# Optimization experiments

Measured on AMD Instinct MI355X. Metric: run time of the kernel, lower is better.

Reference implementation:

```python
import jax, jax.numpy as jnp
import numpy as np

B, L, H, N, NLAYERS = 16, 2048, 256, 64, 4
PRENORM = True


def layer_norm(z, scale, bias, eps=1e-5):
    # z: (B, L, H); normalize over last (feature) axis
    mu = jnp.mean(z, axis=-1, keepdims=True)
    var = jnp.var(z, axis=-1, keepdims=True)
    return (z - mu) * jax.lax.rsqrt(var + eps) * scale + bias


def s4_block(u, log_dt, Alog, Aim, Cre, Cim, D, Wout, bout):
    # u: (B, H, L) -- canonical S4D block: FFT conv + D skip + GELU + GLU linear
    Lq = u.shape[-1]
    dt = jnp.exp(log_dt)[:, None]                      # (H, 1)
    A = -jnp.exp(Alog) + 1j * Aim                      # (H, N)
    C = Cre + 1j * Cim                                 # (H, N)
    dtA = A * dt                                       # (H, N)
    Cd = C * (jnp.exp(dtA) - 1.0) / A                  # ZOH discretization
    vand = jnp.exp(dtA[:, :, None] * jnp.arange(Lq))   # (H, N, L) Vandermonde
    K = 2.0 * jnp.real(jnp.einsum('hn,hnl->hl', Cd, vand))  # (H, L) conv kernel
    n = 2 * Lq
    y = jnp.fft.irfft(jnp.fft.rfft(u, n=n) * jnp.fft.rfft(K, n=n), n=n)[..., :Lq]
    y = y + D[:, None] * u
    y = jax.nn.gelu(y)
    z = jnp.einsum('oh,bhl->bol', Wout, y) + bout[None, :, None]  # (B, 2H, L)
    z1, z2 = jnp.split(z, 2, axis=1)
    return z1 * jax.nn.sigmoid(z2)                     # GLU -> (B, H, L)


def setup_inputs() -> dict:
    key = jax.random.key(0)
    ks = jax.random.split(key, 8)
    x = jax.random.normal(ks[0], (B, L, H), jnp.float32)
    # dt log-uniform in [1e-3, 1e-1]
    log_dt = jnp.log(10.0 ** jax.random.uniform(ks[1], (NLAYERS, H), minval=-3.0, maxval=-1.0)).astype(jnp.float32)
    Alog = jnp.log(0.5 * jnp.ones((NLAYERS, H, N), jnp.float32))
    Aim = jnp.broadcast_to(np.pi * jnp.arange(N, dtype=jnp.float32), (NLAYERS, H, N)).copy()
    Cre = jax.random.normal(ks[2], (NLAYERS, H, N), jnp.float32) * (0.5 ** 0.5)
    Cim = jax.random.normal(ks[3], (NLAYERS, H, N), jnp.float32) * (0.5 ** 0.5)
    D = jax.random.normal(ks[4], (NLAYERS, H), jnp.float32)
    Wout = jax.random.normal(ks[5], (NLAYERS, 2 * H, H), jnp.float32) / jnp.sqrt(jnp.float32(H))
    bout = jnp.zeros((NLAYERS, 2 * H), jnp.float32)
    ln_scale = jnp.ones((NLAYERS, H), jnp.float32)
    ln_bias = jnp.zeros((NLAYERS, H), jnp.float32)
    return dict(x=x, log_dt=log_dt, Alog=Alog, Aim=Aim, Cre=Cre, Cim=Cim, D=D,
                Wout=Wout, bout=bout, ln_scale=ln_scale, ln_bias=ln_bias)


def reference(x, log_dt, Alog, Aim, Cre, Cim, D, Wout, bout, ln_scale, ln_bias):
    # x: (B, L, H); module transposes to (B, H, L) internally
    h = jnp.swapaxes(x, -1, -2)
    for i in range(NLAYERS):
        z = h
        if PRENORM:
            z = jnp.swapaxes(layer_norm(jnp.swapaxes(z, -1, -2), ln_scale[i], ln_bias[i]), -1, -2)
        z = s4_block(z, log_dt[i], Alog[i], Aim[i], Cre[i], Cim[i], D[i], Wout[i], bout[i])
        h = z + h  # dropout is identity in eval mode
        if not PRENORM:
            h = jnp.swapaxes(layer_norm(jnp.swapaxes(h, -1, -2), ln_scale[i], ln_bias[i]), -1, -2)
    return jnp.swapaxes(h, -1, -2)
```

## Files before the change

### kernel.cpp

```cpp
#include <hip/hip_runtime.h>
#include <hip/hip_bf16.h>
#include <math.h>

#define Bq 16
#define Lq 2048
#define Hq 256
#define Nst 64
#define LC 128
#define NC 16
#define NL 4
#define BC 256
#define GK 256
#define PWS 133
#define SZ ((size_t)Bq * Lq * Hq)

typedef __attribute__((ext_vector_type(8))) short short8;
typedef __attribute__((ext_vector_type(4))) float f32x4;
typedef unsigned short u16;
typedef unsigned int u32;

__device__ __forceinline__ u16 f2b(float x) {
  __hip_bfloat16 b = __float2bfloat16(x);
  u16 u; __builtin_memcpy(&u, &b, 2); return u;
}
__device__ __forceinline__ float b2f(u16 u) {
  u32 t = ((u32)u) << 16; float f; __builtin_memcpy(&f, &t, 4); return f;
}
__device__ __forceinline__ void gload16(const void* g, void* l) {
  __builtin_amdgcn_global_load_lds(
      (const __attribute__((address_space(1))) void*)g,
      (__attribute__((address_space(3))) void*)l, 16, 0, 0);
}

__global__ __launch_bounds__(256) void param_k(
    const float* __restrict__ log_dt, const float* __restrict__ Alog,
    const float* __restrict__ Aim, const float* __restrict__ Cre,
    const float* __restrict__ Cim, const float* __restrict__ Dv,
    u16* __restrict__ Vb, u16* __restrict__ TRb, float* __restrict__ wLc) {
  int lh = blockIdx.x;
  int tid = threadIdx.x;
  __shared__ float pwre[32][PWS], pwim[32][PWS];
  __shared__ float cdre[32], cdim[32];
  __shared__ float kacc[LC];
  __shared__ float kts[LC];
  int ln2 = tid & 31, pg = tid >> 5;
  float dlt = expf(log_dt[lh]);

  for (int pass = 0; pass < 2; ++pass) {
    int n = pass * 32 + ln2;
    int gi = lh * Nst + n;
    float ar = -expf(Alog[gi]);
    float ai = Aim[gi];
    float dr = ar * dlt, di = ai * dlt;
    float er = expf(dr); float sn, cs; sincosf(di, &sn, &cs);
    float wr = er * cs, wi = er * sn;
    float p0 = (float)(16 * pg);
    float eb = expf(dr * p0); float sb, cb; sincosf(di * p0, &sb, &cb);
    float pr = eb * cb, pi = eb * sb;
    #pragma unroll
    for (int s = 0; s < 16; ++s) {
      pwre[ln2][16*pg + s] = pr; pwim[ln2][16*pg + s] = pi;
      float t = pr*wr - pi*wi; pi = fmaf(pr, wi, pi*wr); pr = t;
    }
    if (pg == 7) {
      pwre[ln2][128] = pr; pwim[ln2][128] = pi;
      wLc[2*gi] = pr; wLc[2*gi+1] = pi;
    }
    if (pg == 0) {
      float nr = wr - 1.f, ni = wi;
      float d2 = ar*ar + ai*ai;
      float qr = (nr*ar + ni*ai) / d2;
      float qi = (ni*ar - nr*ai) / d2;
      float cr = Cre[gi], ci = Cim[gi];
      cdre[ln2] = cr*qr - ci*qi;
      cdim[ln2] = cr*qi + ci*qr;
    }
    __syncthreads();
    if (tid < LC) {
      float s = 0.f;
      #pragma unroll
      for (int k = 0; k < 32; ++k)
        s = fmaf(cdre[k], pwre[k][tid], fmaf(-cdim[k], pwim[k][tid], s));
      if (pass == 0) kacc[tid] = s;
      else kts[tid] = 2.f * (kacc[tid] + s) + ((tid == 0) ? Dv[lh] : 0.f);
    }
    #pragma unroll
    for (int it = 0; it < 32; ++it) {
      int idx = it * 256 + tid;
      int rl = idx >> 7, j = idx & 127;
      int nl = rl >> 1, im = rl & 1;
      int p = 127 - j;
      float v = im ? pwim[nl][p] : pwre[nl][p];
      Vb[((size_t)lh * 128 + 64*pass + rl) * 128 + j] = f2b(v);
    }
    #pragma unroll
    for (int it = 0; it < 32; ++it) {
      int idx = it * 256 + tid;
      int t = idx >> 6, rl = idx & 63;
      int nl = rl >> 1, im = rl & 1;
      float wpr = pwre[nl][t+1], wpi = pwim[nl][t+1];
      float qr = cdre[nl]*wpr - cdim[nl]*wpi;
      float qi = cdre[nl]*wpi + cdim[nl]*wpr;
      TRb[((size_t)lh * 128 + t) * 256 + 128 + 64*pass + rl] =
          f2b(im ? -2.f*qi : 2.f*qr);
    }
    __syncthreads();
  }
  #pragma unroll
  for (int it = 0; it < 64; ++it) {
    int idx = it * 256 + tid;
    int t = idx >> 7, j = idx & 127;
    TRb[((size_t)lh * 128 + t) * 256 + j] = f2b(j <= t ? kts[t - j] : 0.f);
  }
}

__global__ __launch_bounds__(256) void cvtw_k(
    const float* __restrict__ w, __hip_bfloat16* __restrict__ wb, int n) {
  int i = blockIdx.x * 256 + threadIdx.x;
  if (i < n) wb[i] = __float2bfloat16(w[i]);
}

__global__ __launch_bounds__(512) void lntr_k(
    const float* __restrict__ src, const float* __restrict__ sc,
    const float* __restrict__ bi, u16* __restrict__ zt) {
  int bc = blockIdx.x, jh = blockIdx.y;
  __shared__ u16 Lt[64][Hq + 6];
  int wave = threadIdx.x >> 6, lane = threadIdx.x & 63;
  float4 scv = ((const float4*)sc)[lane];
  float4 biv = ((const float4*)bi)[lane];
  #pragma unroll
  for (int rr = 0; rr < 8; ++rr) {
    int j = wave * 8 + rr;
    size_t row = (size_t)bc * LC + jh * 64 + j;
    const float4 v = ((const float4*)(src + row * Hq))[lane];
    float s  = v.x + v.y + v.z + v.w;
    float s2 = v.x*v.x + v.y*v.y + v.z*v.z + v.w*v.w;
    for (int off = 32; off; off >>= 1) { s += __shfl_down(s, off); s2 += __shfl_down(s2, off); }
    s = __shfl(s, 0); s2 = __shfl(s2, 0);
    float mu = s * (1.f / Hq);
    float var = s2 * (1.f / Hq) - mu * mu;
    float r = rsqrtf(var + 1e-5f);
    u32 w0 = (u32)f2b((v.x - mu) * r * scv.x + biv.x)
           | ((u32)f2b((v.y - mu) * r * scv.y + biv.y) << 16);
    u32 w1 = (u32)f2b((v.z - mu) * r * scv.z + biv.z)
           | ((u32)f2b((v.w - mu) * r * scv.w + biv.w) << 16);
    *(u32*)&Lt[j][4 * lane]     = w0;
    *(u32*)&Lt[j][4 * lane + 2] = w1;
  }
  __syncthreads();
  #pragma unroll
  for (int it = 0; it < 16; ++it) {
    int idx = it * 512 + threadIdx.x;
    int h = idx >> 5, jl = idx & 31;
    u32 lo = Lt[2*jl][h], hi = Lt[2*jl+1][h];
    ((u32*)zt)[((size_t)h * BC + bc) * 64 + jh * 32 + jl] = lo | (hi << 16);
  }
}

__global__ __launch_bounds__(512) void s4core_k(
    const u16* __restrict__ zt, const u16* __restrict__ Vb,
    const u16* __restrict__ TRb, const float* __restrict__ wLc,
    u16* __restrict__ ytb) {
  int h = blockIdx.y;
  int m0 = blockIdx.x * 128;
  __shared__ u16 As[2][128 * 64];
  __shared__ u16 Bs[128 * 64];
  int tid = threadIdx.x;
  int wid = tid >> 6, lane = tid & 63;
  int cl = lane & 15, kq = lane >> 4;
  int wm = wid & 1, wn = wid >> 1;

  const u16* Ab  = zt  + ((size_t)h * BC + m0) * 128;
  const u16* Vbb = Vb  + (size_t)h * 128 * 128;
  const u16* Tbb = TRb + (size_t)h * 128 * 256;

  #pragma unroll
  for (int half = 0; half < 2; ++half)
    #pragma unroll
    for (int q = 0; q < 2; ++q) {
      int idx = q * 512 + tid;
      int r = idx >> 3, ch = idx & 7;
      gload16(Ab + (size_t)r * 128 + half * 64 + ((ch ^ (r & 7)) << 3),
              (char*)As[half] + (size_t)(q * 512 + (tid & ~63)) * 16);
    }

  auto stageB = [&](const u16* base, int stride, int col0) {
    #pragma unroll
    for (int q = 0; q < 2; ++q) {
      int idx = q * 512 + tid;
      int r = idx >> 3, ch = idx & 7;
      gload16(base + (size_t)r * stride + col0 + ((ch ^ (r & 7)) << 3),
              (char*)Bs + (size_t)(q * 512 + (tid & ~63)) * 16);
    }
  };

  f32x4 accS[4][2] = {};
  f32x4 accY[4][2] = {};

  auto mfstep = [&](const u16* Asrc, f32x4 (*acc)[2]) {
    #pragma unroll
    for (int kk = 0; kk < 2; ++kk) {
      short8 a[4], bf[2];
      #pragma unroll
      for (int mi = 0; mi < 4; ++mi) {
        int m = wm * 64 + mi * 16 + cl;
        int ch = (kk * 4 + kq) ^ (m & 7);
        a[mi] = *(const short8*)(Asrc + m * 64 + ch * 8);
      }
      #pragma unroll
      for (int ni = 0; ni < 2; ++ni) {
        int n = wn * 32 + ni * 16 + cl;
        int ch = (kk * 4 + kq) ^ (n & 7);
        bf[ni] = *(const short8*)(Bs + n * 64 + ch * 8);
      }
      #pragma unroll
      for (int mi = 0; mi < 4; ++mi)
        #pragma unroll
        for (int ni = 0; ni < 2; ++ni)
          acc[mi][ni] = __builtin_amdgcn_mfma_f32_16x16x32_bf16(
              a[mi], bf[ni], acc[mi][ni], 0, 0, 0);
    }
  };

  stageB(Vbb, 128, 0);   __syncthreads();
  mfstep(As[0], accS);   __syncthreads();
  stageB(Vbb, 128, 64);  __syncthreads();
  mfstep(As[1], accS);   __syncthreads();
  stageB(Tbb, 256, 0);   __syncthreads();
  mfstep(As[0], accY);   __syncthreads();
  stageB(Tbb, 256, 64);  __syncthreads();
  mfstep(As[1], accY);

  float sgn = (cl & 1) ? 1.f : -1.f;
  #pragma unroll
  for (int ni = 0; ni < 2; ++ni) {
    int n = (wn * 32 + ni * 16 + cl) >> 1;
    float wr = wLc[2 * (h * Nst + n)];
    float wi = wLc[2 * (h * Nst + n) + 1];
    float swi = sgn * wi;
    #pragma unroll
    for (int mi = 0; mi < 4; ++mi) {
      float carry = 0.f;
      #pragma unroll
      for (int c = 0; c < NC; ++c) {
        float part = __shfl_xor(carry, 1);
        float a_used = accS[mi][ni][c & 3];
        float Sc = fmaf(wr, carry, fmaf(swi, part, a_used));
        if (kq == (c >> 2)) accS[mi][ni][c & 3] = carry;
        carry = __shfl(Sc, ((c >> 2) << 4) + cl);
      }
    }
  }

  __syncthreads();
  #pragma unroll
  for (int mi = 0; mi < 4; ++mi)
    #pragma unroll
    for (int ni = 0; ni < 2; ++ni) {
      int colv = wn * 32 + ni * 16 + cl;
      int half = colv >> 6, cv = colv & 63;
      #pragma unroll
      for (int r = 0; r < 4; ++r) {
        int m = wm * 64 + mi * 16 + kq * 4 + r;
        As[half][m * 64 + (((cv >> 3) ^ (m & 7)) << 3) + (cv & 7)] =
            f2b(accS[mi][ni][r]);
      }
    }
  stageB(Tbb, 256, 128);  __syncthreads();
  mfstep(As[0], accY);    __syncthreads();
  stageB(Tbb, 256, 192);  __syncthreads();
  mfstep(As[1], accY);

  #pragma unroll
  for (int mi = 0; mi < 4; ++mi)
    #pragma unroll
    for (int ni = 0; ni < 2; ++ni) {
      int t = wn * 32 + ni * 16 + cl;
      #pragma unroll
      for (int r = 0; r < 4; ++r) {
        int row = m0 + wm * 64 + mi * 16 + kq * 4 + r;
        float x = accY[mi][ni][r];
        float inner = 0.7978845608028654f * fmaf(0.044715f, x*x*x, x);
        float g = 0.5f * x * (1.f + tanhf(inner));
        ytb[((size_t)h * BC + row) * LC + t] = f2b(g);
      }
    }
}

__global__ __launch_bounds__(256) void trB_k(
    const u16* __restrict__ ytb, u16* __restrict__ ybb) {
  int bc = blockIdx.x;
  int h0 = blockIdx.y * 64;
  __shared__ float Lt[128][65];
  const u16* src = ytb + ((size_t)h0 * BC + bc) * LC;
  for (int it = 0; it < 16; ++it) {
    int idx = it * 256 + threadIdx.x;
    int hh = idx >> 6, tl = idx & 63;
    u32 v = *(const u32*)(src + (size_t)hh * BC * LC + 2 * tl);
    Lt[2*tl][hh]   = b2f((u16)(v & 0xffff));
    Lt[2*tl+1][hh] = b2f((u16)(v >> 16));
  }
  __syncthreads();
  for (int it = 0; it < 16; ++it) {
    int idx = it * 256 + threadIdx.x;
    int t = idx >> 5, hl = idx & 31;
    u32 lo = f2b(Lt[t][2*hl]);
    u32 hi = f2b(Lt[t][2*hl+1]);
    ((u32*)ybb)[((size_t)bc * LC + t) * (Hq / 2) + h0 / 2 + hl] = lo | (hi << 16);
  }
}

__global__ __launch_bounds__(256) void gemm_k(
    const __hip_bfloat16* __restrict__ ybb, const __hip_bfloat16* __restrict__ Wb,
    const float* __restrict__ bout, const float* __restrict__ rsrc,
    float* __restrict__ hb) {
  __shared__ __hip_bfloat16 As[128 * 64];
  __shared__ __hip_bfloat16 Bs[128 * 64];
  int tid = threadIdx.x;
  int m0 = blockIdx.x * 128;
  int ot = blockIdx.y;
  int wid = tid >> 6, lane = tid & 63;
  int cl = lane & 15, kq = lane >> 4;
  f32x4 acc[2][8] = {};
  for (int kt = 0; kt < GK / 64; ++kt) {
    int k0 = kt * 64;
    #pragma unroll
    for (int q = 0; q < 4; ++q) {
      int idx = q * 256 + tid;
      int r = idx >> 3, ch = idx & 7;
      const __hip_bfloat16* sA =
          ybb + (size_t)(m0 + r) * GK + k0 + ((ch ^ (r & 7)) << 3);
      gload16(sA, (char*)As + (size_t)(q * 256 + (tid & ~63)) * 16);
      int wrow = ot * 64 + r + ((r >= 64) ? 192 : 0);
      const __hip_bfloat16* sB =
          Wb + (size_t)wrow * GK + k0 + ((ch ^ (r & 7)) << 3);
      gload16(sB, (char*)Bs + (size_t)(q * 256 + (tid & ~63)) * 16);
    }
    __syncthreads();
    #pragma unroll
    for (int kk = 0; kk < 2; ++kk) {
      short8 a[2], bfr[8];
      #pragma unroll
      for (int mi = 0; mi < 2; ++mi) {
        int m = wid * 32 + mi * 16 + cl;
        int ch = (kk * 4 + kq) ^ (m & 7);
        a[mi] = *(const short8*)(As + m * 64 + ch * 8);
      }
      #pragma unroll
      for (int ni = 0; ni < 8; ++ni) {
        int n = ni * 16 + cl;
        int ch = (kk * 4 + kq) ^ (n & 7);
        bfr[ni] = *(const short8*)(Bs + n * 64 + ch * 8);
      }
      #pragma unroll
      for (int mi = 0; mi < 2; ++mi)
        #pragma unroll
        for (int ni = 0; ni < 8; ++ni)
          acc[mi][ni] = __builtin_amdgcn_mfma_f32_16x16x32_bf16(
              a[mi], bfr[ni], acc[mi][ni], 0, 0, 0);
    }
    __syncthreads();
  }
  #pragma unroll
  for (int mi = 0; mi < 2; ++mi) {
    #pragma unroll
    for (int ni = 0; ni < 4; ++ni) {
      int o1 = ot * 64 + ni * 16 + cl;
      float b1 = bout[o1], b2 = bout[o1 + 256];
      #pragma unroll
      for (int r = 0; r < 4; ++r) {
        int row = m0 + wid * 32 + mi * 16 + kq * 4 + r;
        float z1 = acc[mi][ni][r] + b1;
        float z2 = acc[mi][ni + 4][r] + b2;
        float g = z1 / (1.f + expf(-z2));
        size_t idx = (size_t)row * Hq + o1;
        hb[idx] = rsrc[idx] + g;
      }
    }
  }
}

extern "C" void kernel_launch(void* const* d_in, const int* in_sizes, int n_in,
                              void* d_out, int out_size, void* d_ws, size_t ws_size,
                              hipStream_t stream) {
  (void)in_sizes; (void)n_in; (void)out_size; (void)ws_size;
  const float* x      = (const float*)d_in[0];
  const float* log_dt = (const float*)d_in[1];
  const float* Alog   = (const float*)d_in[2];
  const float* Aim    = (const float*)d_in[3];
  const float* Cre    = (const float*)d_in[4];
  const float* Cim    = (const float*)d_in[5];
  const float* Dv     = (const float*)d_in[6];
  const float* Wout   = (const float*)d_in[7];
  const float* bout   = (const float*)d_in[8];
  const float* lns    = (const float*)d_in[9];
  const float* lnb    = (const float*)d_in[10];

  float* hb = (float*)d_out;
  float* p  = (float*)d_ws;
  u16* zt  = (u16*)p; p += SZ/2;
  u16* ytb = (u16*)p; p += SZ/2;
  u16* ybb = (u16*)p; p += SZ/2;
  u16* Vb  = (u16*)p; p += SZ;
  u16* TRb = (u16*)p; p += 2*SZ;
  u16* Wb  = (u16*)p; p += (NL*2*Hq*Hq)/2;
  float* wLc = p;  p += NL*2*Hq*Nst;

  cvtw_k<<<(NL*2*Hq*Hq)/256, 256, 0, stream>>>(Wout, (__hip_bfloat16*)Wb, NL*2*Hq*Hq);
  param_k<<<NL*Hq, 256, 0, stream>>>(log_dt, Alog, Aim, Cre, Cim, Dv, Vb, TRb, wLc);

  for (int i = 0; i < NL; ++i) {
    const float* src = (i == 0) ? x : hb;
    lntr_k<<<dim3(BC, 2), 512, 0, stream>>>(src, lns + i*Hq, lnb + i*Hq, zt);
    s4core_k<<<dim3(2, Hq), 512, 0, stream>>>(
        zt, Vb + (size_t)i * Hq * 128 * 128, TRb + (size_t)i * Hq * 128 * 256,
        wLc + (size_t)i * 2 * Hq * Nst, ytb);
    trB_k<<<dim3(BC, 4), 256, 0, stream>>>(ytb, ybb);
    gemm_k<<<dim3((Bq*Lq)/128, 4), 256, 0, stream>>>(
        (const __hip_bfloat16*)ybb,
        (const __hip_bfloat16*)(Wb + (size_t)i * 2 * Hq * Hq),
        bout + (size_t)i*2*Hq, src, hb);
  }
}
```

Before: 306.9 us.

## Double-buffer B tiles in s4core and vectorize parameter-kernel bf16 stores

In s4core_k, B tiles are now double-buffered in shared memory, so the next tile's global-to-LDS load is issued before the MFMA step on the current tile. This cuts the number of barriers and overlaps load latency with compute. In param_k, the Vandermonde and Toeplitz/TR bf16 matrix writes are packed into 16-byte vector stores instead of scalar 2-byte stores. The cost is 16KB more LDS per block, which may lower occupancy, and the reordered barriers must still order the async LDS writes correctly.

Result: no change. 306.9 us (-0.0%).

```diff
diff --git a/kernel.cpp b/kernel.cpp
--- a/kernel.cpp
+++ b/kernel.cpp
@@ -16,6 +16,7 @@
 
 typedef __attribute__((ext_vector_type(8))) short short8;
 typedef __attribute__((ext_vector_type(4))) float f32x4;
+typedef __attribute__((ext_vector_type(4))) unsigned int u32x4;
 typedef unsigned short u16;
 typedef unsigned int u32;
 
@@ -85,32 +86,52 @@
       else kts[tid] = 2.f * (kacc[tid] + s) + ((tid == 0) ? Dv[lh] : 0.f);
     }
     #pragma unroll
-    for (int it = 0; it < 32; ++it) {
+    for (int it = 0; it < 4; ++it) {
       int idx = it * 256 + tid;
-      int rl = idx >> 7, j = idx & 127;
+      int rl = idx >> 4, g = idx & 15;
       int nl = rl >> 1, im = rl & 1;
-      int p = 127 - j;
-      float v = im ? pwim[nl][p] : pwre[nl][p];
-      Vb[((size_t)lh * 128 + 64*pass + rl) * 128 + j] = f2b(v);
-    }
-    #pragma unroll
-    for (int it = 0; it < 32; ++it) {
+      const float* row = im ? pwim[nl] : pwre[nl];
+      int pj = 127 - 8 * g;
+      u32x4 v;
+      #pragma unroll
+      for (int e = 0; e < 4; ++e) {
+        u32 lo = f2b(row[pj - 2*e]);
+        u32 hi = f2b(row[pj - 2*e - 1]);
+        v[e] = lo | (hi << 16);
+      }
+      *(u32x4*)&Vb[((size_t)lh * 128 + 64*pass + rl) * 128 + 8*g] = v;
+    }
+    #pragma unroll
+    for (int it = 0; it < 4; ++it) {
       int idx = it * 256 + tid;
-      int t = idx >> 6, rl = idx & 63;
-      int nl = rl >> 1, im = rl & 1;
-      float wpr = pwre[nl][t+1], wpi = pwim[nl][t+1];
-      float qr = cdre[nl]*wpr - cdim[nl]*wpi;
-      float qi = cdre[nl]*wpi + cdim[nl]*wpr;
-      TRb[((size_t)lh * 128 + t) * 256 + 128 + 64*pass + rl] =
-          f2b(im ? -2.f*qi : 2.f*qr);
+      int t = idx >> 3, g = idx & 7;
+      u32x4 v;
+      #pragma unroll
+      for (int k = 0; k < 4; ++k) {
+        int nl = 4*g + k;
+        float wpr = pwre[nl][t+1], wpi = pwim[nl][t+1];
+        float qr = cdre[nl]*wpr - cdim[nl]*wpi;
+        float qi = cdre[nl]*wpi + cdim[nl]*wpr;
+        v[k] = (u32)f2b(2.f * qr) | ((u32)f2b(-2.f * qi) << 16);
+      }
+      *(u32x4*)&TRb[((size_t)lh * 128 + t) * 256 + 128 + 64*pass + 8*g] = v;
     }
     __syncthreads();
   }
   #pragma unroll
-  for (int it = 0; it < 64; ++it) {
+  for (int it = 0; it < 8; ++it) {
     int idx = it * 256 + tid;
-    int t = idx >> 7, j = idx & 127;
-    TRb[((size_t)lh * 128 + t) * 256 + j] = f2b(j <= t ? kts[t - j] : 0.f);
+    int t = idx >> 4, g = idx & 15;
+    int j0 = 8 * g;
+    u32x4 v;
+    #pragma unroll
+    for (int e = 0; e < 4; ++e) {
+      int j = j0 + 2*e;
+      u32 lo = (j     <= t) ? (u32)f2b(kts[t - j])     : 0u;
+      u32 hi = (j + 1 <= t) ? (u32)f2b(kts[t - j - 1]) : 0u;
+      v[e] = lo | (hi << 16);
+    }
+    *(u32x4*)&TRb[((size_t)lh * 128 + t) * 256 + j0] = v;
   }
 }
 
@@ -164,7 +185,7 @@
   int h = blockIdx.y;
   int m0 = blockIdx.x * 128;
   __shared__ u16 As[2][128 * 64];
-  __shared__ u16 Bs[128 * 64];
+  __shared__ u16 Bs[2][128 * 64];
   int tid = threadIdx.x;
   int wid = tid >> 6, lane = tid & 63;
   int cl = lane & 15, kq = lane >> 4;
@@ -184,20 +205,20 @@
               (char*)As[half] + (size_t)(q * 512 + (tid & ~63)) * 16);
     }
 
-  auto stageB = [&](const u16* base, int stride, int col0) {
+  auto stageB = [&](const u16* base, int stride, int col0, u16* dst) {
     #pragma unroll
     for (int q = 0; q < 2; ++q) {
       int idx = q * 512 + tid;
       int r = idx >> 3, ch = idx & 7;
       gload16(base + (size_t)r * stride + col0 + ((ch ^ (r & 7)) << 3),
-              (char*)Bs + (size_t)(q * 512 + (tid & ~63)) * 16);
+              (char*)dst + (size_t)(q * 512 + (tid & ~63)) * 16);
     }
   };
 
   f32x4 accS[4][2] = {};
   f32x4 accY[4][2] = {};
 
-  auto mfstep = [&](const u16* Asrc, f32x4 (*acc)[2]) {
+  auto mfstep = [&](const u16* Asrc, const u16* Bsrc, f32x4 (*acc)[2]) {
     #pragma unroll
     for (int kk = 0; kk < 2; ++kk) {
       short8 a[4], bf[2];
@@ -211,7 +232,7 @@
       for (int ni = 0; ni < 2; ++ni) {
         int n = wn * 32 + ni * 16 + cl;
         int ch = (kk * 4 + kq) ^ (n & 7);
-        bf[ni] = *(const short8*)(Bs + n * 64 + ch * 8);
+        bf[ni] = *(const short8*)(Bsrc + n * 64 + ch * 8);
       }
       #pragma unroll
       for (int mi = 0; mi < 4; ++mi)
@@ -222,14 +243,16 @@
     }
   };
 
-  stageB(Vbb, 128, 0);   __syncthreads();
-  mfstep(As[0], accS);   __syncthreads();
-  stageB(Vbb, 128, 64);  __syncthreads();
-  mfstep(As[1], accS);   __syncthreads();
-  stageB(Tbb, 256, 0);   __syncthreads();
-  mfstep(As[0], accY);   __syncthreads();
-  stageB(Tbb, 256, 64);  __syncthreads();
-  mfstep(As[1], accY);
+  stageB(Vbb, 128, 0, Bs[0]);
+  __syncthreads();
+  stageB(Vbb, 128, 64, Bs[1]);
+  mfstep(As[0], Bs[0], accS);  __syncthreads();
+  stageB(Tbb, 256, 0, Bs[0]);
+  mfstep(As[1], Bs[1], accS);  __syncthreads();
+  stageB(Tbb, 256, 64, Bs[1]);
+  mfstep(As[0], Bs[0], accY);  __syncthreads();
+  stageB(Tbb, 256, 128, Bs[0]);
+  mfstep(As[1], Bs[1], accY);  __syncthreads();
 
   float sgn = (cl & 1) ? 1.f : -1.f;
   #pragma unroll
@@ -252,7 +275,6 @@
     }
   }
 
-  __syncthreads();
   #pragma unroll
   for (int mi = 0; mi < 4; ++mi)
     #pragma unroll
@@ -266,10 +288,10 @@
             f2b(accS[mi][ni][r]);
       }
     }
-  stageB(Tbb, 256, 128);  __syncthreads();
-  mfstep(As[0], accY);    __syncthreads();
-  stageB(Tbb, 256, 192);  __syncthreads();
-  mfstep(As[1], accY);
+  stageB(Tbb, 256, 192, Bs[1]);
+  __syncthreads();
+  mfstep(As[0], Bs[0], accY);
+  mfstep(As[1], Bs[1], accY);
 
   #pragma unroll
   for (int mi = 0; mi < 4; ++mi)
```
